# Kernel optimization log

Hardware: AMD Instinct MI355X
Metric: run time of the kernel (lower is better)

## Reference

```python
import jax, jax.numpy as jnp
import numpy as np

VOCAB = 100000
EMB = 128
B = 16384
C = 20
N = 20


def setup_inputs() -> dict:
    key = jax.random.key(0)
    k1, k2, k3, k4, k5 = jax.random.split(key, 5)
    initrange = 1.0 / EMB
    return {
        "pos_target": jax.random.randint(k1, (B,), 0, VOCAB),
        "pos_contexts": jax.random.randint(k2, (B, C), 0, VOCAB),
        "pos_negatives": jax.random.randint(k3, (B, N), 0, VOCAB),
        "context_table": jax.random.uniform(k4, (VOCAB, EMB), jnp.float32, -initrange, initrange),
        "output_table": jax.random.uniform(k5, (VOCAB, EMB), jnp.float32, -initrange, initrange),
    }


def reference(pos_target, pos_contexts, pos_negatives, context_table, output_table):
    # gather + sum over context window: [B, C, D] -> [B, D]
    mean_contexts = jnp.sum(context_table[pos_contexts], axis=1)
    emb_target = output_table[pos_target]           # [B, D]
    emb_negs = output_table[pos_negatives]          # [B, N, D]

    # positive objective: dot(mean_contexts, emb_target) per row
    pos_score = jnp.clip(jnp.sum(mean_contexts * emb_target, axis=1), -10.0, 10.0)
    objective = -jax.nn.log_sigmoid(pos_score)      # [B]

    # negative objective: bmm [B,N,D] x [B,D] -> [B,N]
    neg_score = jnp.clip(jnp.einsum("bnd,bd->bn", emb_negs, mean_contexts), -10.0, 10.0)
    neg_objective = -jnp.sum(jax.nn.log_sigmoid(-neg_score), axis=1)  # [B]

    return jnp.mean(objective + neg_objective)
```

## Files before the change

### kernel.cpp

```cpp
#include <hip/hip_runtime.h>
#include <math.h>

#define VOCAB 100000
#define EMB   128
#define BATCH 16384
#define CTX   20
#define NEG   20
#define NSCORE (NEG + 1)

__device__ __forceinline__ float dot4(float4 a, float4 b) {
    return fmaf(a.x, b.x, fmaf(a.y, b.y, fmaf(a.z, b.z, a.w * b.w)));
}

__device__ __forceinline__ float fast_softplus(float x) {
    return __logf(1.0f + __expf(x));
}

__global__ __launch_bounds__(256, 4) void cbow_loss_kernel(
    const int*   __restrict__ pos_target,
    const int*   __restrict__ pos_contexts,
    const int*   __restrict__ pos_negatives,
    const float* __restrict__ context_table,
    const float* __restrict__ output_table,
    float*       __restrict__ out)
{
    const int tid  = threadIdx.x;
    const int lane = tid & 63;
    const int wave = tid >> 6;
    const int half = lane >> 5;
    const int sub  = lane & 31;

    const int row = blockIdx.x * 8 + wave * 2 + half;

    const float4* ctab = (const float4*)context_table;
    const float4* otab = (const float4*)output_table;

    float4 acc = make_float4(0.f, 0.f, 0.f, 0.f);
    const int cbase = row * CTX;
#pragma unroll
    for (int c = 0; c < CTX; ++c) {
        const int idx = pos_contexts[cbase + c];
        const float4 v = ctab[idx * 32 + sub];
        acc.x += v.x; acc.y += v.y; acc.z += v.z; acc.w += v.w;
    }

    int sidx[NSCORE];
    sidx[0] = pos_target[row];
    const int nbase = row * NEG;
#pragma unroll
    for (int n = 0; n < NEG; ++n) sidx[1 + n] = pos_negatives[nbase + n];

    float part[NSCORE];
#pragma unroll
    for (int g = 0; g < 3; ++g) {
        float4 vb[7];
#pragma unroll
        for (int j = 0; j < 7; ++j) vb[j] = otab[sidx[g * 7 + j] * 32 + sub];
#pragma unroll
        for (int j = 0; j < 7; ++j) part[g * 7 + j] = dot4(acc, vb[j]);
    }

#pragma unroll
    for (int s = 16; s >= 1; s >>= 1) {
#pragma unroll
        for (int n = 0; n < NSCORE; ++n) part[n] += __shfl_xor(part[n], s);
    }

    float ps = fminf(fmaxf(part[0], -10.f), 10.f);
    float loss = fast_softplus(-ps);
#pragma unroll
    for (int n = 1; n < NSCORE; ++n) {
        float ns = fminf(fmaxf(part[n], -10.f), 10.f);
        loss += fast_softplus(ns);
    }

    __shared__ float sdata[8];
    if (sub == 0) sdata[wave * 2 + half] = loss;
    __syncthreads();
    if (tid == 0) {
        float s = 0.f;
#pragma unroll
        for (int i = 0; i < 8; ++i) s += sdata[i];
        atomicAdd(out, s * (1.0f / (float)BATCH));
    }
}

extern "C" void kernel_launch(void* const* d_in, const int* in_sizes, int n_in,
                              void* d_out, int out_size, void* d_ws, size_t ws_size,
                              hipStream_t stream) {
    const int*   pos_target    = (const int*)d_in[0];
    const int*   pos_contexts  = (const int*)d_in[1];
    const int*   pos_negatives = (const int*)d_in[2];
    const float* context_table = (const float*)d_in[3];
    const float* output_table  = (const float*)d_in[4];
    float* out = (float*)d_out;

    hipMemsetAsync(out, 0, sizeof(float), stream);

    const int rows_per_block = 8;
    const int grid = BATCH / rows_per_block;
    cbow_loss_kernel<<<grid, 256, 0, stream>>>(
        pos_target, pos_contexts, pos_negatives, context_table, output_table, out);
}
```

Before: 151.4 us.

## Map one full wave per row with float2 loads and all gathers issued upfront

After: 171.6 us. +13.4%, slower.

```diff
diff --git a/kernel.cpp b/kernel.cpp
--- a/kernel.cpp
+++ b/kernel.cpp
@@ -7,10 +7,6 @@
 #define CTX   20
 #define NEG   20
 #define NSCORE (NEG + 1)
-
-__device__ __forceinline__ float dot4(float4 a, float4 b) {
-    return fmaf(a.x, b.x, fmaf(a.y, b.y, fmaf(a.z, b.z, a.w * b.w)));
-}
 
 __device__ __forceinline__ float fast_softplus(float x) {
     return __logf(1.0f + __expf(x));
@@ -27,41 +23,37 @@
     const int tid  = threadIdx.x;
     const int lane = tid & 63;
     const int wave = tid >> 6;
-    const int half = lane >> 5;
-    const int sub  = lane & 31;
 
-    const int row = blockIdx.x * 8 + wave * 2 + half;
+    const int row = __builtin_amdgcn_readfirstlane(blockIdx.x * 4 + wave);
 
-    const float4* ctab = (const float4*)context_table;
-    const float4* otab = (const float4*)output_table;
+    const float2* ctab = (const float2*)context_table;
+    const float2* otab = (const float2*)output_table;
 
-    float4 acc = make_float4(0.f, 0.f, 0.f, 0.f);
-    const int cbase = row * CTX;
+    int cidx[CTX], sidx[NSCORE];
 #pragma unroll
-    for (int c = 0; c < CTX; ++c) {
-        const int idx = pos_contexts[cbase + c];
-        const float4 v = ctab[idx * 32 + sub];
-        acc.x += v.x; acc.y += v.y; acc.z += v.z; acc.w += v.w;
-    }
+    for (int c = 0; c < CTX; ++c) cidx[c] = pos_contexts[row * CTX + c];
+    sidx[0] = pos_target[row];
+#pragma unroll
+    for (int n = 0; n < NEG; ++n) sidx[1 + n] = pos_negatives[row * NEG + n];
 
-    int sidx[NSCORE];
-    sidx[0] = pos_target[row];
-    const int nbase = row * NEG;
+    float2 cv[CTX];
+    float2 sv[NSCORE];
 #pragma unroll
-    for (int n = 0; n < NEG; ++n) sidx[1 + n] = pos_negatives[nbase + n];
+    for (int c = 0; c < CTX; ++c) cv[c] = ctab[(size_t)cidx[c] * 64 + lane];
+#pragma unroll
+    for (int n = 0; n < NSCORE; ++n) sv[n] = otab[(size_t)sidx[n] * 64 + lane];
+
+    float2 acc = make_float2(0.f, 0.f);
+#pragma unroll
+    for (int c = 0; c < CTX; ++c) { acc.x += cv[c].x; acc.y += cv[c].y; }
 
     float part[NSCORE];
 #pragma unroll
-    for (int g = 0; g < 3; ++g) {
-        float4 vb[7];
-#pragma unroll
-        for (int j = 0; j < 7; ++j) vb[j] = otab[sidx[g * 7 + j] * 32 + sub];
-#pragma unroll
-        for (int j = 0; j < 7; ++j) part[g * 7 + j] = dot4(acc, vb[j]);
-    }
+    for (int n = 0; n < NSCORE; ++n)
+        part[n] = fmaf(acc.x, sv[n].x, acc.y * sv[n].y);
 
 #pragma unroll
-    for (int s = 16; s >= 1; s >>= 1) {
+    for (int s = 32; s >= 1; s >>= 1) {
 #pragma unroll
         for (int n = 0; n < NSCORE; ++n) part[n] += __shfl_xor(part[n], s);
     }
@@ -74,13 +66,11 @@
         loss += fast_softplus(ns);
     }
 
-    __shared__ float sdata[8];
-    if (sub == 0) sdata[wave * 2 + half] = loss;
+    __shared__ float sdata[4];
+    if (lane == 0) sdata[wave] = loss;
     __syncthreads();
     if (tid == 0) {
-        float s = 0.f;
-#pragma unroll
-        for (int i = 0; i < 8; ++i) s += sdata[i];
+        float s = sdata[0] + sdata[1] + sdata[2] + sdata[3];
         atomicAdd(out, s * (1.0f / (float)BATCH));
     }
 }
@@ -97,7 +87,7 @@
 
     hipMemsetAsync(out, 0, sizeof(float), stream);
 
-    const int rows_per_block = 8;
+    const int rows_per_block = 4;
     const int grid = BATCH / rows_per_block;
     cbow_loss_kernel<<<grid, 256, 0, stream>>>(
         pos_target, pos_contexts, pos_negatives, context_table, output_table, out);
```
